# Optimization experiments

Measured on AMD Instinct MI355X. Metric: run time of the kernel, lower is better.

Reference implementation:

```python
import jax, jax.numpy as jnp
import numpy as np

NEG_SLOPE = 0.2  # PyG GATConv default leaky_relu slope


def gat_conv(x, src, dst, n, W, a_src, a_dst, b):
    """Single-head PyG GATConv (self-loops already included in src/dst)."""
    h = x @ W                                  # [N, F]
    alpha_s = h @ a_src                        # [N]
    alpha_d = h @ a_dst                        # [N]
    e = jax.nn.leaky_relu(alpha_s[src] + alpha_d[dst], NEG_SLOPE)  # [E]
    m = jax.ops.segment_max(e, dst, num_segments=n)
    e = jnp.exp(e - m[dst])
    s = jax.ops.segment_sum(e, dst, num_segments=n)
    alpha = e / s[dst]                         # softmax over incoming edges
    out = jax.ops.segment_sum(alpha[:, None] * h[src], dst, num_segments=n)
    return out + b


def setup_inputs() -> dict:
    key = jax.random.key(0)
    ks = jax.random.split(key, 12)
    N, E = 8192, 262144
    IN, H, OUT, K = 512, 128, 64, 16
    x = jax.random.normal(ks[0], (N, IN), dtype=jnp.float32)
    edge_index = jax.random.randint(ks[1], (2, E), 0, N, dtype=jnp.int32)
    def glorot(k, shape):
        lim = np.sqrt(6.0 / (shape[0] + shape[-1]))
        return jax.random.uniform(k, shape, jnp.float32, -lim, lim)
    return {
        "x": x,
        "edge_index": edge_index,
        "W1": glorot(ks[2], (IN, H)),
        "a_src1": glorot(ks[3], (H,)),
        "a_dst1": glorot(ks[4], (H,)),
        "b1": jnp.zeros((H,), jnp.float32),
        "W2": glorot(ks[5], (H, OUT)),
        "a_src2": glorot(ks[6], (OUT,)),
        "a_dst2": glorot(ks[7], (OUT,)),
        "b2": jnp.zeros((OUT,), jnp.float32),
        "centers": glorot(ks[8], (K, OUT)),
    }


def reference(x, edge_index, W1, a_src1, a_dst1, b1, W2, a_src2, a_dst2, b2, centers):
    n = x.shape[0]
    # add self loops (PyG GATConv default add_self_loops=True)
    loop = jnp.arange(n, dtype=edge_index.dtype)
    src = jnp.concatenate([edge_index[0], loop])
    dst = jnp.concatenate([edge_index[1], loop])
    h = jax.nn.elu(gat_conv(x, src, dst, n, W1, a_src1, a_dst1, b1))
    z = gat_conv(h, src, dst, n, W2, a_src2, a_dst2, b2)       # [N, D]
    A_pred = jax.nn.sigmoid(z @ z.T)                            # [N, N]
    # Student-t soft assignment: [N, K]
    d2 = jnp.sum((z[:, None, :] - centers[None, :, :]) ** 2, axis=2)
    q = 1.0 / (1.0 + d2)
    q = q / jnp.sum(q, axis=1, keepdims=True)
    return (z, A_pred, q)
```

## Files before the change

### kernel.cpp

```cpp
#include <hip/hip_runtime.h>
#include <hip/hip_bf16.h>

typedef __bf16 v8bf __attribute__((ext_vector_type(8)));
typedef unsigned short v8us __attribute__((ext_vector_type(8)));
typedef float  v4f  __attribute__((ext_vector_type(4)));

__device__ __forceinline__ float lrelu02(float x){ return x > 0.f ? x : 0.2f*x; }

__device__ __forceinline__ unsigned short f2bf_rn(float f){
  unsigned int u = __float_as_uint(f);
  u += 0x7fffu + ((u >> 16) & 1u);
  return (unsigned short)(u >> 16);
}
__device__ __forceinline__ float bf2f(unsigned short h){
  return __uint_as_float(((unsigned int)h) << 16);
}

union BF8cast { v8us u; v8bf b; };

__global__ void hist_kernel(const int* __restrict__ dst, int* counts, int E){
  int i = blockIdx.x*blockDim.x + threadIdx.x;
  if (i < E) atomicAdd(&counts[dst[i]], 1);
}

__global__ void scan_kernel(const int* __restrict__ counts, int* ptr, int* cursor, int n){
  __shared__ int sd[1024];
  int t = threadIdx.x;
  int base = t*8;
  int v[8]; int s = 0;
  #pragma unroll
  for (int i = 0; i < 8; ++i){ int x = (base+i < n) ? counts[base+i] : 0; v[i] = x; s += x; }
  sd[t] = s; __syncthreads();
  for (int off = 1; off < 1024; off <<= 1){
    int x = (t >= off) ? sd[t-off] : 0;
    __syncthreads();
    sd[t] += x;
    __syncthreads();
  }
  int run = sd[t] - s;
  #pragma unroll
  for (int i = 0; i < 8; ++i){
    if (base+i < n){ ptr[base+i] = run; cursor[base+i] = run; run += v[i]; }
  }
  if (t == 1023) ptr[n] = run;
}

__global__ void scatter_kernel(const int* __restrict__ src, const int* __restrict__ dst,
                               int* cursor, int* csr_src, int E){
  int i = blockIdx.x*blockDim.x + threadIdx.x;
  if (i < E){
    int p = atomicAdd(&cursor[dst[i]], 1);
    csr_src[p] = src[i];
  }
}

__global__ void prep_kernel(const float* __restrict__ W1,
    unsigned short* wth, unsigned short* wtl, int* counts, int nw, int n){
  int i = blockIdx.x*blockDim.x + threadIdx.x;
  if (i < nw){
    int k = i >> 7, c = i & 127;
    float f = W1[i];
    unsigned short h = f2bf_rn(f);
    wth[c*512 + k] = h;
    wtl[c*512 + k] = f2bf_rn(f - bf2f(h));
  } else if (i < nw + n){
    counts[i - nw] = 0;
  }
}

__global__ __launch_bounds__(128) void gemm1_fused(const float* __restrict__ x,
    const unsigned short* __restrict__ wth, const unsigned short* __restrict__ wtl,
    const float* __restrict__ avs, const float* __restrict__ avd,
    float* __restrict__ h1, float* __restrict__ as_out, float* __restrict__ ad_out){
  const int lane = threadIdx.x & 63;
  const int wave = threadIdx.x >> 6;
  const int i0 = blockIdx.x*32 + wave*16;
  const int r = lane & 15, q = lane >> 4;
  const float* xr = x + (size_t)(i0 + r)*512;
  v4f acc[8];
  #pragma unroll
  for (int c = 0; c < 8; ++c) acc[c] = (v4f){0.f,0.f,0.f,0.f};
  for (int kt = 0; kt < 16; ++kt){
    int k = kt*32 + q*8;
    v4f xa = *reinterpret_cast<const v4f*>(xr + k);
    v4f xb = *reinterpret_cast<const v4f*>(xr + k + 4);
    v8us ahu, alu;
    #pragma unroll
    for (int j = 0; j < 8; ++j){
      float f = (j < 4) ? xa[j] : xb[j-4];
      unsigned short hh = f2bf_rn(f);
      ahu[j] = hh;
      alu[j] = f2bf_rn(f - bf2f(hh));
    }
    BF8cast ch; ch.u = ahu;
    BF8cast cl; cl.u = alu;
    v8bf ah = ch.b, al = cl.b;
    #pragma unroll
    for (int ct = 0; ct < 8; ++ct){
      v8bf bh = *reinterpret_cast<const v8bf*>(wth + (size_t)(ct*16 + r)*512 + k);
      v8bf bl = *reinterpret_cast<const v8bf*>(wtl + (size_t)(ct*16 + r)*512 + k);
      acc[ct] = __builtin_amdgcn_mfma_f32_16x16x32_bf16(ah, bh, acc[ct], 0,0,0);
      acc[ct] = __builtin_amdgcn_mfma_f32_16x16x32_bf16(al, bh, acc[ct], 0,0,0);
      acc[ct] = __builtin_amdgcn_mfma_f32_16x16x32_bf16(ah, bl, acc[ct], 0,0,0);
    }
  }
  #pragma unroll
  for (int ct = 0; ct < 8; ++ct)
    #pragma unroll
    for (int t = 0; t < 4; ++t)
      h1[(size_t)(i0 + q*4 + t)*128 + ct*16 + r] = acc[ct][t];
  float sa[4] = {0.f,0.f,0.f,0.f}, da[4] = {0.f,0.f,0.f,0.f};
  #pragma unroll
  for (int ct = 0; ct < 8; ++ct){
    float ws = avs[ct*16 + r], wd = avd[ct*16 + r];
    #pragma unroll
    for (int t = 0; t < 4; ++t){ sa[t] += acc[ct][t]*ws; da[t] += acc[ct][t]*wd; }
  }
  #pragma unroll
  for (int off = 1; off < 16; off <<= 1){
    #pragma unroll
    for (int t = 0; t < 4; ++t){
      sa[t] += __shfl_xor(sa[t], off);
      da[t] += __shfl_xor(da[t], off);
    }
  }
  if (r == 0){
    #pragma unroll
    for (int t = 0; t < 4; ++t){
      as_out[i0 + q*4 + t] = sa[t];
      ad_out[i0 + q*4 + t] = da[t];
    }
  }
}

__global__ void gat_agg1(const float* __restrict__ h, const float* __restrict__ as,
                         const float* __restrict__ ad, const int* __restrict__ ptr,
                         const int* __restrict__ csr_src, const float* __restrict__ bias,
                         float* __restrict__ out, int n){
  const int F = 128;
  int wid = (blockIdx.x*blockDim.x + threadIdx.x) >> 6;
  int lane = threadIdx.x & 63;
  if (wid >= n) return;
  const int v = wid;
  const int beg = ptr[v], end = ptr[v+1];
  const float adv = ad[v];
  const float asv = as[v];
  float m = lrelu02(asv + adv);
  for (int j = beg + lane; j < end; j += 64)
    m = fmaxf(m, lrelu02(as[csr_src[j]] + adv));
  for (int o = 32; o; o >>= 1) m = fmaxf(m, __shfl_xor(m, o));
  const int half = lane >> 5, l32 = lane & 31;
  v4f acc = (v4f){0.f,0.f,0.f,0.f};
  float wself = __expf(lrelu02(asv + adv) - m);
  float ssum = (lane == 0) ? wself : 0.f;
  if (half == 0){
    v4f hv = *reinterpret_cast<const v4f*>(h + (size_t)v*F + l32*4);
    acc += hv * wself;
  }
  for (int b0 = beg; b0 < end; b0 += 64){
    int j = b0 + lane;
    float wv = 0.f; int sv = 0;
    if (j < end){
      sv = csr_src[j];
      wv = __expf(lrelu02(as[sv] + adv) - m);
      ssum += wv;
    }
    int cnt = min(64, end - b0);
    for (int t = 0; t < cnt; t += 2){
      int idx = t + half;
      float wt = __shfl(wv, idx);
      int   st = __shfl(sv, idx);
      if (idx >= cnt){ wt = 0.f; st = v; }
      v4f hv = *reinterpret_cast<const v4f*>(h + (size_t)st*F + l32*4);
      acc += hv * wt;
    }
  }
  for (int o = 32; o; o >>= 1) ssum += __shfl_xor(ssum, o);
  #pragma unroll
  for (int c = 0; c < 4; ++c) acc[c] += __shfl_xor(acc[c], 32);
  if (half == 0){
    float inv = 1.f / ssum;
    v4f bv = *reinterpret_cast<const v4f*>(bias + l32*4);
    v4f rr;
    #pragma unroll
    for (int c = 0; c < 4; ++c){
      float r0 = acc[c]*inv + bv[c];
      rr[c] = r0 > 0.f ? r0 : __expf(r0) - 1.f;
    }
    *reinterpret_cast<v4f*>(out + (size_t)v*F + l32*4) = rr;
  }
}

template<int BM,int BN,int BK,int TM,int TN>
__global__ __launch_bounds__(256) void gemm2_fused(const float* __restrict__ A,
    const float* __restrict__ B, float* __restrict__ C, int M, int N, int K,
    const float* __restrict__ avs, const float* __restrict__ avd,
    float* __restrict__ as_out, float* __restrict__ ad_out){
  __shared__ float As[BK][BM+1];
  __shared__ float Bs[BK][BN+1];
  __shared__ float reds[BM][17];
  __shared__ float redd[BM][17];
  const int tid = threadIdx.x;
  const int tx = tid % (BN/TN);
  const int ty = tid / (BN/TN);
  const int brow = blockIdx.y*BM;
  const int bcol = blockIdx.x*BN;
  float acc[TM][TN] = {};
  for (int k0 = 0; k0 < K; k0 += BK){
    for (int i = tid; i < BM*BK; i += 256){
      int m = i / BK, kk = i % BK;
      As[kk][m] = A[(size_t)(brow+m)*K + k0 + kk];
    }
    for (int i = tid; i < BK*BN; i += 256){
      int kk = i / BN, nn = i % BN;
      Bs[kk][nn] = B[(size_t)(k0+kk)*N + bcol + nn];
    }
    __syncthreads();
    #pragma unroll
    for (int kk = 0; kk < BK; ++kk){
      float a[TM], b[TN];
      #pragma unroll
      for (int m = 0; m < TM; ++m) a[m] = As[kk][ty*TM+m];
      #pragma unroll
      for (int n = 0; n < TN; ++n) b[n] = Bs[kk][tx*TN+n];
      #pragma unroll
      for (int m = 0; m < TM; ++m)
        #pragma unroll
        for (int n = 0; n < TN; ++n) acc[m][n] += a[m]*b[n];
    }
    __syncthreads();
  }
  float ps[TM] = {}, pd[TM] = {};
  #pragma unroll
  for (int m = 0; m < TM; ++m){
    #pragma unroll
    for (int n = 0; n < TN; ++n){
      float c = acc[m][n];
      C[(size_t)(brow+ty*TM+m)*N + bcol+tx*TN+n] = c;
      float s = avs[bcol+tx*TN+n], d = avd[bcol+tx*TN+n];
      ps[m] += c*s; pd[m] += c*d;
    }
  }
  #pragma unroll
  for (int m = 0; m < TM; ++m){
    reds[ty*TM+m][tx] = ps[m];
    redd[ty*TM+m][tx] = pd[m];
  }
  __syncthreads();
  if (tid < BM){
    float s = 0.f, d = 0.f;
    #pragma unroll
    for (int k = 0; k < BN/TN; ++k){ s += reds[tid][k]; d += redd[tid][k]; }
    as_out[brow + tid] = s;
    ad_out[brow + tid] = d;
  }
}

__global__ void gat_agg2_fused(const float* __restrict__ h, const float* __restrict__ as,
                               const float* __restrict__ ad, const int* __restrict__ ptr,
                               const int* __restrict__ csr_src, const float* __restrict__ bias,
                               const float* __restrict__ centers,
                               float* __restrict__ z_out, unsigned short* __restrict__ zhi,
                               unsigned short* __restrict__ zlo, float* __restrict__ qout,
                               int n, int K){
  const int F = 64;
  int wid = (blockIdx.x*blockDim.x + threadIdx.x) >> 6;
  int lane = threadIdx.x & 63;
  if (wid >= n) return;
  const int v = wid;
  const int beg = ptr[v], end = ptr[v+1];
  const float adv = ad[v];
  const float asv = as[v];
  float m = lrelu02(asv + adv);
  for (int j = beg + lane; j < end; j += 64)
    m = fmaxf(m, lrelu02(as[csr_src[j]] + adv));
  for (int o = 32; o; o >>= 1) m = fmaxf(m, __shfl_xor(m, o));
  const int qr = lane >> 4, l16 = lane & 15;
  v4f acc = (v4f){0.f,0.f,0.f,0.f};
  float wself = __expf(lrelu02(asv + adv) - m);
  float ssum = (lane == 0) ? wself : 0.f;
  if (qr == 0){
    v4f hv = *reinterpret_cast<const v4f*>(h + (size_t)v*F + l16*4);
    acc += hv * wself;
  }
  for (int b0 = beg; b0 < end; b0 += 64){
    int j = b0 + lane;
    float wv = 0.f; int sv = 0;
    if (j < end){
      sv = csr_src[j];
      wv = __expf(lrelu02(as[sv] + adv) - m);
      ssum += wv;
    }
    int cnt = min(64, end - b0);
    for (int t = 0; t < cnt; t += 4){
      int idx = t + qr;
      float wt = __shfl(wv, idx);
      int   st = __shfl(sv, idx);
      if (idx >= cnt){ wt = 0.f; st = v; }
      v4f hv = *reinterpret_cast<const v4f*>(h + (size_t)st*F + l16*4);
      acc += hv * wt;
    }
  }
  for (int o = 32; o; o >>= 1) ssum += __shfl_xor(ssum, o);
  #pragma unroll
  for (int c = 0; c < 4; ++c){
    acc[c] += __shfl_xor(acc[c], 16);
    acc[c] += __shfl_xor(acc[c], 32);
  }
  int srcLane = lane >> 2;
  float c0 = __shfl(acc[0], srcLane);
  float c1 = __shfl(acc[1], srcLane);
  float c2 = __shfl(acc[2], srcLane);
  float c3 = __shfl(acc[3], srcLane);
  int sel = lane & 3;
  float av = sel == 0 ? c0 : sel == 1 ? c1 : sel == 2 ? c2 : c3;
  float r0 = av / ssum + bias[lane];
  z_out[(size_t)v*F + lane] = r0;
  unsigned short hh = f2bf_rn(r0);
  zhi[(size_t)v*F + lane] = hh;
  zlo[(size_t)v*F + lane] = f2bf_rn(r0 - bf2f(hh));
  float myq = 0.f, tot = 0.f;
  for (int k = 0; k < K; ++k){
    float d = r0 - centers[k*F + lane];
    float d2 = d*d;
    for (int o = 32; o; o >>= 1) d2 += __shfl_xor(d2, o);
    float qq = 1.f / (1.f + d2);
    if (lane == k) myq = qq;
    tot += qq;
  }
  if (lane < K) qout[(size_t)v*K + lane] = myq / tot;
}

__device__ __forceinline__ v8bf ldz(const unsigned short* z, int node, int k){
  return *reinterpret_cast<const v8bf*>(z + ((size_t)node << 6) + k);
}

__global__ __launch_bounds__(256) void apred_kernel(const unsigned short* __restrict__ zhi,
    const unsigned short* __restrict__ zlo, float* __restrict__ out, int N){
  __shared__ float tile[4][16][68];
  const int lane = threadIdx.x & 63;
  const int wave = threadIdx.x >> 6;
  const int i0 = blockIdx.y*64 + wave*16;
  const int j0 = blockIdx.x*64;
  const int r = lane & 15, q = lane >> 4;
  const int arow = i0 + r;
  v8bf ahi0 = ldz(zhi, arow,      q*8);
  v8bf ahi1 = ldz(zhi, arow, 32 + q*8);
  v8bf alo0 = ldz(zlo, arow,      q*8);
  v8bf alo1 = ldz(zlo, arow, 32 + q*8);
  #pragma unroll
  for (int c = 0; c < 4; ++c){
    int brow = j0 + c*16 + r;
    v8bf bhi0 = ldz(zhi, brow,      q*8);
    v8bf bhi1 = ldz(zhi, brow, 32 + q*8);
    v8bf blo0 = ldz(zlo, brow,      q*8);
    v8bf blo1 = ldz(zlo, brow, 32 + q*8);
    v4f acc = {0.f,0.f,0.f,0.f};
    acc = __builtin_amdgcn_mfma_f32_16x16x32_bf16(ahi0, bhi0, acc, 0,0,0);
    acc = __builtin_amdgcn_mfma_f32_16x16x32_bf16(ahi1, bhi1, acc, 0,0,0);
    acc = __builtin_amdgcn_mfma_f32_16x16x32_bf16(ahi0, blo0, acc, 0,0,0);
    acc = __builtin_amdgcn_mfma_f32_16x16x32_bf16(ahi1, blo1, acc, 0,0,0);
    acc = __builtin_amdgcn_mfma_f32_16x16x32_bf16(alo0, bhi0, acc, 0,0,0);
    acc = __builtin_amdgcn_mfma_f32_16x16x32_bf16(alo1, bhi1, acc, 0,0,0);
    #pragma unroll
    for (int t = 0; t < 4; ++t){
      float e = __expf(-acc[t]);
      tile[wave][q*4 + t][c*16 + r] = __builtin_amdgcn_rcpf(1.f + e);
    }
  }
  #pragma unroll
  for (int t = 0; t < 4; ++t){
    int row = t*4 + (lane >> 4);
    int col = (lane & 15)*4;
    v4f vv = *reinterpret_cast<v4f*>(&tile[wave][row][col]);
    __builtin_nontemporal_store(vv, reinterpret_cast<v4f*>(out + (size_t)(i0 + row)*N + j0 + col));
  }
}

extern "C" void kernel_launch(void* const* d_in, const int* in_sizes, int n_in,
                              void* d_out, int out_size, void* d_ws, size_t ws_size,
                              hipStream_t stream) {
  const float* x      = (const float*)d_in[0];
  const int*   ei     = (const int*)  d_in[1];
  const float* W1     = (const float*)d_in[2];
  const float* a_src1 = (const float*)d_in[3];
  const float* a_dst1 = (const float*)d_in[4];
  const float* b1     = (const float*)d_in[5];
  const float* W2     = (const float*)d_in[6];
  const float* a_src2 = (const float*)d_in[7];
  const float* a_dst2 = (const float*)d_in[8];
  const float* b2     = (const float*)d_in[9];
  const float* cent   = (const float*)d_in[10];

  const int H   = in_sizes[3];
  const int OUTF= in_sizes[7];
  const int INF = in_sizes[2] / H;
  const int N   = in_sizes[0] / INF;
  const int E   = in_sizes[1] / 2;
  const int K   = in_sizes[10] / OUTF;

  const int* e_src = ei;
  const int* e_dst = ei + E;

  char* wsp = (char*)d_ws;
  auto alloc = [&](size_t b)->void*{ void* p = (void*)wsp; wsp += (b + 255) & ~(size_t)255; return p; };
  int* counts   = (int*)alloc((size_t)N*4);
  int* ptr      = (int*)alloc((size_t)(N+1)*4);
  int* cursor   = (int*)alloc((size_t)N*4);
  int* csr_src  = (int*)alloc((size_t)E*4);
  float* as1    = (float*)alloc((size_t)N*4);
  float* ad1    = (float*)alloc((size_t)N*4);
  float* as2    = (float*)alloc((size_t)N*4);
  float* ad2    = (float*)alloc((size_t)N*4);
  unsigned short* zhi = (unsigned short*)alloc((size_t)N*OUTF*2);
  unsigned short* zlo = (unsigned short*)alloc((size_t)N*OUTF*2);
  unsigned short* wth = (unsigned short*)alloc((size_t)INF*H*2);
  unsigned short* wtl = (unsigned short*)alloc((size_t)INF*H*2);

  float* out_f  = (float*)d_out;
  float* z_out  = out_f;
  float* ap_out = out_f + (size_t)N*OUTF;
  float* q_out  = ap_out + (size_t)N*N;
  float* h1  = ap_out;
  float* h2  = h1 + (size_t)N*H;
  float* h2w = h2 + (size_t)N*H;

  const int wavesPerGrid = (N*64 + 255)/256;
  const int nw = INF*H;

  prep_kernel<<<(nw + N + 255)/256, 256, 0, stream>>>(W1, wth, wtl, counts, nw, N);
  hist_kernel<<<(E+255)/256, 256, 0, stream>>>(e_dst, counts, E);
  scan_kernel<<<1, 1024, 0, stream>>>(counts, ptr, cursor, N);
  scatter_kernel<<<(E+255)/256, 256, 0, stream>>>(e_src, e_dst, cursor, csr_src, E);
  gemm1_fused<<<N/32, 128, 0, stream>>>(x, wth, wtl, a_src1, a_dst1, h1, as1, ad1);
  gat_agg1<<<wavesPerGrid, 256, 0, stream>>>(h1, as1, ad1, ptr, csr_src, b1, h2, N);
  gemm2_fused<64,64,16,4,4><<<dim3(OUTF/64, N/64), 256, 0, stream>>>(h2, W2, h2w, N, OUTF, H,
                                                                     a_src2, a_dst2, as2, ad2);
  gat_agg2_fused<<<wavesPerGrid, 256, 0, stream>>>(h2w, as2, ad2, ptr, csr_src, b2, cent,
                                                   z_out, zhi, zlo, q_out, N, K);
  apred_kernel<<<dim3(N/64, N/64), 256, 0, stream>>>(zhi, zlo, ap_out, N);
}
```

Measured before the change: 546.1 us.

## Cache first edge chunk in aggregation and widen A_pred tiles with XCD swizzle

Result: faster. 528.2 us (-3.3%).

```diff
diff --git a/kernel.cpp b/kernel.cpp
--- a/kernel.cpp
+++ b/kernel.cpp
@@ -143,23 +143,39 @@
   if (wid >= n) return;
   const int v = wid;
   const int beg = ptr[v], end = ptr[v+1];
+  const int deg = end - beg;
   const float adv = ad[v];
   const float asv = as[v];
-  float m = lrelu02(asv + adv);
-  for (int j = beg + lane; j < end; j += 64)
+  const float eself = lrelu02(asv + adv);
+  int sv0 = v; float e0 = -3.4e38f;
+  if (lane < deg){ sv0 = csr_src[beg + lane]; e0 = lrelu02(as[sv0] + adv); }
+  float m = fmaxf(eself, e0);
+  for (int j = beg + 64 + lane; j < end; j += 64)
     m = fmaxf(m, lrelu02(as[csr_src[j]] + adv));
   for (int o = 32; o; o >>= 1) m = fmaxf(m, __shfl_xor(m, o));
+  float wv0 = (lane < deg) ? __expf(e0 - m) : 0.f;
+  float wself = __expf(eself - m);
+  float ssum = wv0 + ((lane == 0) ? wself : 0.f);
   const int half = lane >> 5, l32 = lane & 31;
   v4f acc = (v4f){0.f,0.f,0.f,0.f};
-  float wself = __expf(lrelu02(asv + adv) - m);
-  float ssum = (lane == 0) ? wself : 0.f;
   if (half == 0){
     v4f hv = *reinterpret_cast<const v4f*>(h + (size_t)v*F + l32*4);
     acc += hv * wself;
   }
-  for (int b0 = beg; b0 < end; b0 += 64){
+  {
+    int cnt = min(64, deg);
+    for (int t = 0; t < cnt; t += 2){
+      int idx = t + half;
+      float wt = __shfl(wv0, idx);
+      int   st = __shfl(sv0, idx);
+      if (idx >= cnt){ wt = 0.f; st = v; }
+      v4f hv = *reinterpret_cast<const v4f*>(h + (size_t)st*F + l32*4);
+      acc += hv * wt;
+    }
+  }
+  for (int b0 = beg + 64; b0 < end; b0 += 64){
     int j = b0 + lane;
-    float wv = 0.f; int sv = 0;
+    float wv = 0.f; int sv = v;
     if (j < end){
       sv = csr_src[j];
       wv = __expf(lrelu02(as[sv] + adv) - m);
@@ -269,23 +285,39 @@
   if (wid >= n) return;
   const int v = wid;
   const int beg = ptr[v], end = ptr[v+1];
+  const int deg = end - beg;
   const float adv = ad[v];
   const float asv = as[v];
-  float m = lrelu02(asv + adv);
-  for (int j = beg + lane; j < end; j += 64)
+  const float eself = lrelu02(asv + adv);
+  int sv0 = v; float e0 = -3.4e38f;
+  if (lane < deg){ sv0 = csr_src[beg + lane]; e0 = lrelu02(as[sv0] + adv); }
+  float m = fmaxf(eself, e0);
+  for (int j = beg + 64 + lane; j < end; j += 64)
     m = fmaxf(m, lrelu02(as[csr_src[j]] + adv));
   for (int o = 32; o; o >>= 1) m = fmaxf(m, __shfl_xor(m, o));
+  float wv0 = (lane < deg) ? __expf(e0 - m) : 0.f;
+  float wself = __expf(eself - m);
+  float ssum = wv0 + ((lane == 0) ? wself : 0.f);
   const int qr = lane >> 4, l16 = lane & 15;
   v4f acc = (v4f){0.f,0.f,0.f,0.f};
-  float wself = __expf(lrelu02(asv + adv) - m);
-  float ssum = (lane == 0) ? wself : 0.f;
   if (qr == 0){
     v4f hv = *reinterpret_cast<const v4f*>(h + (size_t)v*F + l16*4);
     acc += hv * wself;
   }
-  for (int b0 = beg; b0 < end; b0 += 64){
+  {
+    int cnt = min(64, deg);
+    for (int t = 0; t < cnt; t += 4){
+      int idx = t + qr;
+      float wt = __shfl(wv0, idx);
+      int   st = __shfl(sv0, idx);
+      if (idx >= cnt){ wt = 0.f; st = v; }
+      v4f hv = *reinterpret_cast<const v4f*>(h + (size_t)st*F + l16*4);
+      acc += hv * wt;
+    }
+  }
+  for (int b0 = beg + 64; b0 < end; b0 += 64){
     int j = b0 + lane;
-    float wv = 0.f; int sv = 0;
+    float wv = 0.f; int sv = v;
     if (j < end){
       sv = csr_src[j];
       wv = __expf(lrelu02(as[sv] + adv) - m);
@@ -337,11 +369,17 @@
 
 __global__ __launch_bounds__(256) void apred_kernel(const unsigned short* __restrict__ zhi,
     const unsigned short* __restrict__ zlo, float* __restrict__ out, int N){
-  __shared__ float tile[4][16][68];
+  __shared__ float tile[4][16][132];
+  const int nwg = gridDim.x * gridDim.y;
+  int wg = blockIdx.y * gridDim.x + blockIdx.x;
+  int cpx = nwg >> 3;
+  int swz = (wg & 7) * cpx + (wg >> 3);
+  int by = swz / gridDim.x;
+  int bx = swz - by * gridDim.x;
   const int lane = threadIdx.x & 63;
   const int wave = threadIdx.x >> 6;
-  const int i0 = blockIdx.y*64 + wave*16;
-  const int j0 = blockIdx.x*64;
+  const int i0 = by*64 + wave*16;
+  const int j0 = bx*128;
   const int r = lane & 15, q = lane >> 4;
   const int arow = i0 + r;
   v8bf ahi0 = ldz(zhi, arow,      q*8);
@@ -349,7 +387,7 @@
   v8bf alo0 = ldz(zlo, arow,      q*8);
   v8bf alo1 = ldz(zlo, arow, 32 + q*8);
   #pragma unroll
-  for (int c = 0; c < 4; ++c){
+  for (int c = 0; c < 8; ++c){
     int brow = j0 + c*16 + r;
     v8bf bhi0 = ldz(zhi, brow,      q*8);
     v8bf bhi1 = ldz(zhi, brow, 32 + q*8);
@@ -369,9 +407,9 @@
     }
   }
   #pragma unroll
-  for (int t = 0; t < 4; ++t){
-    int row = t*4 + (lane >> 4);
-    int col = (lane & 15)*4;
+  for (int t = 0; t < 8; ++t){
+    int row = t*2 + (lane >> 5);
+    int col = (lane & 31)*4;
     v4f vv = *reinterpret_cast<v4f*>(&tile[wave][row][col]);
     __builtin_nontemporal_store(vv, reinterpret_cast<v4f*>(out + (size_t)(i0 + row)*N + j0 + col));
   }
@@ -438,5 +476,5 @@
                                                                      a_src2, a_dst2, as2, ad2);
   gat_agg2_fused<<<wavesPerGrid, 256, 0, stream>>>(h2w, as2, ad2, ptr, csr_src, b2, cent,
                                                    z_out, zhi, zlo, q_out, N, K);
-  apred_kernel<<<dim3(N/64, N/64), 256, 0, stream>>>(zhi, zlo, ap_out, N);
-}
+  apred_kernel<<<dim3(N/128, N/64), 256, 0, stream>>>(zhi, zlo, ap_out, N);
+}
```
